# Kernel tuning notes

Hardware: AMD Instinct MI355X
Metric: run time of the kernel (lower is better)

## Reference

```python
import jax, jax.numpy as jnp
import numpy as np


def _pairwise_adj(x):
    # exp(-||xi - xj||^2), shape [B, N, N]
    inner = -2.0 * jnp.einsum('bnd,bmd->bnm', x, x)
    sq = jnp.sum(x * x, axis=-1, keepdims=True)
    return jnp.exp(-(sq + inner + jnp.swapaxes(sq, 1, 2)))


def _knn_adj(adj, k):
    # keep top-k weights per row, zero elsewhere
    vals, idx = jax.lax.top_k(adj, k)
    b = jnp.arange(adj.shape[0])[:, None, None]
    n = jnp.arange(adj.shape[1])[None, :, None]
    return jnp.zeros_like(adj).at[b, n, idx].set(vals)


def _laplacian(adj):
    # normalized Laplacian L = I - D^-1/2 A D^-1/2
    d = jnp.sum(adj, axis=-1)
    dinv = jnp.where(d > 0, 1.0 / jnp.sqrt(d), 0.0)
    norm_adj = dinv[:, :, None] * adj * dinv[:, None, :]
    return jnp.eye(adj.shape[1], dtype=adj.dtype) - norm_adj


def _cheb_conv(x, L, W, b):
    # Chebyshev polynomial graph conv: sum_k T_k(L) x W_k + b
    K = W.shape[0]
    x0 = x
    out = jnp.einsum('bnf,fo->bno', x0, W[0])
    if K > 1:
        x1 = jnp.matmul(L, x0)
        out = out + jnp.einsum('bnf,fo->bno', x1, W[1])
        for kk in range(2, K):
            x2 = 2.0 * jnp.matmul(L, x1) - x0
            out = out + jnp.einsum('bnf,fo->bno', x2, W[kk])
            x0, x1 = x1, x2
    return out + b


def setup_inputs() -> dict:
    key = jax.random.key(0)
    ks = jax.random.split(key, 4)
    B, N, Fin, Fout, K, C = 16, 2048, 6, 128, 6, 40
    x = jax.random.normal(ks[0], (B, N, Fin), dtype=jnp.float32)
    sccs = jax.random.randint(ks[1], (B, 64, 16), 0, N)  # unused in one_layer branch
    W1 = jax.random.normal(ks[2], (K, Fin, Fout), dtype=jnp.float32) * 0.05
    b1 = jnp.zeros((Fout,), dtype=jnp.float32)
    fc_w = jax.random.normal(ks[3], (Fout, C), dtype=jnp.float32) * 0.05
    fc_b = jnp.zeros((C,), dtype=jnp.float32)
    return {"x": x, "k": 40, "batch_size": B, "num_points": N,
            "sccs": sccs, "W1": W1, "b1": b1, "fc_w": fc_w, "fc_b": fc_b}


def reference(x, k, batch_size, num_points, sccs, W1, b1, fc_w, fc_b):
    # graph built under no_grad in the original -> stop_gradient here
    L = jax.lax.stop_gradient(_laplacian(_knn_adj(_pairwise_adj(x), k)))
    out = jax.nn.relu(_cheb_conv(x, L, W1, b1))           # [B, N, 128]
    # reg_prior: ||out^T L out||_F ** 2
    M = jnp.einsum('bnf,bnm,bmg->bfg', out, L, out)       # [B, 128, 128]
    reg = jnp.sum(M * M)
    pooled = jnp.max(out, axis=1)                         # [B, 128]
    logits = pooled @ fc_w + fc_b                         # [B, class_num]
    return logits, reg
```

## Files before the change

### kernel.cpp

```cpp
#include <hip/hip_runtime.h>
#include <math.h>

#define BB   16
#define NN   2048
#define FIN  6
#define FOUT 128
#define KCH  6
#define KNN  40
#define NCLS 40

__global__ __launch_bounds__(512) void knn_kernel(const float* __restrict__ x,
                                                  int* __restrict__ topi,
                                                  float* __restrict__ topv,
                                                  float* __restrict__ dinv)
{
    __shared__ __align__(16) float xs[FIN][NN];
    __shared__ unsigned int   hist[8][64];
    __shared__ unsigned int   ck[8][64];
    __shared__ unsigned short ci[8][64];
    __shared__ unsigned int   ccnt[8];

    int bb   = blockIdx.x >> 5;
    int i0   = (blockIdx.x & 31) * 64;
    int t    = threadIdx.x;
    int lane = t & 63;
    int wv   = t >> 6;

    const float* xb = x + (size_t)bb * NN * FIN;
    for (int idx = t; idx < NN * FIN; idx += 512) {
        int j = idx / FIN, f = idx - j * FIN;
        xs[f][j] = xb[idx];
    }
    __syncthreads();

    for (int rr = 0; rr < 8; ++rr) {
        int i   = i0 + wv * 8 + rr;
        int row = bb * NN + i;

        float xi0 = xs[0][i], xi1 = xs[1][i], xi2 = xs[2][i],
              xi3 = xs[3][i], xi4 = xs[4][i], xi5 = xs[5][i];

        float d[32];
#pragma unroll
        for (int uu = 0; uu < 8; ++uu) {
            int j4 = uu * 64 + lane;
            float4 p0 = ((const float4*)xs[0])[j4];
            float4 p1 = ((const float4*)xs[1])[j4];
            float4 p2 = ((const float4*)xs[2])[j4];
            float4 p3 = ((const float4*)xs[3])[j4];
            float4 p4 = ((const float4*)xs[4])[j4];
            float4 p5 = ((const float4*)xs[5])[j4];
#define DNE(E, C)                                                                \
            { float q0 = p0.C - xi0, q1 = p1.C - xi1, q2 = p2.C - xi2,           \
                    q3 = p3.C - xi3, q4 = p4.C - xi4, q5 = p5.C - xi5;           \
              d[uu * 4 + E] = fmaf(q5,q5, fmaf(q4,q4, fmaf(q3,q3,                \
                              fmaf(q2,q2, fmaf(q1,q1, q0*q0)))));  }
            DNE(0, x) DNE(1, y) DNE(2, z) DNE(3, w)
#undef DNE
        }

        float lo = 0.0f, invw = 16.0f;
        int base = 0, pivot = 127;

        for (int pass = 0; pass < 6; ++pass) {
            hist[wv][lane] = 0u;
#pragma unroll
            for (int u = 0; u < 32; ++u) {
                float dv = d[u];
                if (dv >= lo) {
                    int bin = (int)((dv - lo) * invw);
                    if (bin < 128)
                        atomicAdd(&hist[wv][bin >> 1], 1u << ((bin & 1) << 4));
                }
            }
            unsigned int h = hist[wv][lane];
            int b0 = (int)(h & 0xFFFFu), b1 = (int)(h >> 16);
            int s = b0 + b1;
            int incl = s;
#pragma unroll
            for (int off = 1; off < 64; off <<= 1) {
                int up = __shfl_up(incl, off, 64);
                if (lane >= off) incl += up;
            }
            int total = __shfl(incl, 63, 64);

            if (base + total < KNN) {
                base += total;
                lo   += 128.0f / invw;
                invw *= 0.5f;
                continue;
            }

            unsigned long long ball = __ballot(base + incl >= KNN);
            int pl = __ffsll(ball) - 1;
            int p_ = 0, cb_ = 0, cs_ = 0;
            if (lane == pl) {
                int cbefore = base + incl - s;
                if (cbefore + b0 >= KNN) { p_ = pl * 2;     cb_ = cbefore;      cs_ = cbefore + b0; }
                else                     { p_ = pl * 2 + 1; cb_ = cbefore + b0; cs_ = cbefore + b0 + b1; }
            }
            pivot    = __shfl(p_, pl, 64);
            int cumb = __shfl(cb_, pl, 64);
            int csel = __shfl(cs_, pl, 64);

            if (csel <= 64) break;

            lo   = lo + (float)pivot / invw;
            invw *= 128.0f;
            base = cumb;
        }

        if (lane == 0) ccnt[wv] = 0u;
#pragma unroll
        for (int u = 0; u < 32; ++u) {
            int ib = (int)((d[u] - lo) * invw);
            if (ib <= pivot) {
                unsigned int slot = atomicAdd(&ccnt[wv], 1u);
                if (slot < 64u) {
                    ck[wv][slot] = __float_as_uint(d[u]);
                    ci[wv][slot] = (unsigned short)((u >> 2) * 256 + (lane << 2) + (u & 3));
                }
            }
        }
        unsigned int c = ccnt[wv];
        if (c > 64u) c = 64u;

        unsigned int kk = (lane < (int)c) ? ck[wv][lane] : 0xFFFFFFFFu;
        int          id = (lane < (int)c) ? (int)ci[wv][lane] : -1;

        int rank = 0;
        int cI = (int)c;
        for (int m = 0; m < cI; ++m) {
            unsigned int km = __shfl(kk, m, 64);
            rank += (km < kk || (km == kk && m < lane)) ? 1 : 0;
        }

        float ev = 0.0f;
        if (rank < KNN) {
            ev = expf(-__uint_as_float(kk));
            topv[(size_t)row * KNN + rank] = ev;
            topi[(size_t)row * KNN + rank] = id;
        }
        float ssum = ev;
#pragma unroll
        for (int off = 32; off; off >>= 1) ssum += __shfl_xor(ssum, off, 64);
        if (lane == 0) dinv[row] = 1.0f / sqrtf(ssum);
    }
}

__global__ void weight_kernel(const int* __restrict__ topi,
                              const float* __restrict__ topv,
                              const float* __restrict__ dinv,
                              float* __restrict__ wnrm)
{
    int idx = blockIdx.x * 256 + threadIdx.x;
    if (idx >= BB * NN * KNN) return;
    int row = idx / KNN;
    int b   = row >> 11;
    int j   = topi[idx];
    wnrm[idx] = topv[idx] * dinv[row] * dinv[b * NN + j];
}

__global__ __launch_bounds__(192) void cheb_apply(const float* __restrict__ xin,
                                                  const float* __restrict__ xsub,
                                                  float* __restrict__ xout,
                                                  const int* __restrict__ topi,
                                                  const float* __restrict__ wnrm,
                                                  float scale)
{
    __shared__ int   si[32 * KNN];
    __shared__ float sw[32 * KNN];
    int r0 = blockIdx.x * 32;
    int t  = threadIdx.x;
    for (int l = t; l < 32 * KNN; l += 192) {
        si[l] = topi[(size_t)r0 * KNN + l];
        sw[l] = wnrm[(size_t)r0 * KNN + l];
    }
    __syncthreads();

    int rl = t / FIN, f = t - rl * FIN;
    int r  = r0 + rl;
    int b  = r >> 11;
    const float* xbase = xin + (size_t)b * NN * FIN + f;
    const int*   sip = si + rl * KNN;
    const float* swp = sw + rl * KNN;
    float a = xin[(size_t)r * FIN + f];
#pragma unroll 8
    for (int s = 0; s < KNN; ++s)
        a = fmaf(-swp[s], xbase[(size_t)sip[s] * FIN], a);
    a *= scale;
    if (xsub) a -= xsub[(size_t)r * FIN + f];
    xout[(size_t)r * FIN + f] = a;
}

__global__ __launch_bounds__(512) void chebout_kernel(const float* __restrict__ x,
                                                      const float* __restrict__ xks,
                                                      const float* __restrict__ W1,
                                                      const float* __restrict__ b1,
                                                      float* __restrict__ outb)
{
    __shared__ float W1s[KCH * FIN * FOUT];
    __shared__ float b1s[FOUT];
    __shared__ float xk[4][KCH * FIN];
    int r0 = blockIdx.x * 4;
    int t  = threadIdx.x;
    for (int l = t; l < KCH * FIN * FOUT; l += 512) W1s[l] = W1[l];
    if (t < FOUT) b1s[t] = b1[t];
    if (t < 4 * KCH * FIN) {
        int rl = t / (KCH * FIN), kf = t % (KCH * FIN);
        int k = kf / FIN, f = kf % FIN;
        int r = r0 + rl;
        xk[rl][kf] = (k == 0) ? x[(size_t)r * FIN + f]
                              : xks[(size_t)(k - 1) * BB * NN * FIN + (size_t)r * FIN + f];
    }
    __syncthreads();
    int rl = t >> 7, fo = t & 127;
    float acc = b1s[fo];
#pragma unroll
    for (int kf = 0; kf < KCH * FIN; ++kf)
        acc = fmaf(xk[rl][kf], W1s[kf * FOUT + fo], acc);
    outb[(size_t)(r0 + rl) * FOUT + fo] = fmaxf(acc, 0.0f);
}

__global__ __launch_bounds__(128) void lout_kernel(const float* __restrict__ outb,
                                                   const int* __restrict__ topi,
                                                   const float* __restrict__ wnrm,
                                                   float* __restrict__ lout)
{
    int id = blockIdx.x;
    int q  = id >> 3;
    int bb = (id & 7) + 8 * (q >> 11);
    int i  = q & 2047;
    int r  = bb * NN + i;
    int t  = threadIdx.x;
    __shared__ int   si[KNN];
    __shared__ float sw[KNN];
    if (t < KNN) { si[t] = topi[(size_t)r * KNN + t]; sw[t] = wnrm[(size_t)r * KNN + t]; }
    __syncthreads();
    const float* ob = outb + (size_t)bb * NN * FOUT;
    float acc = outb[(size_t)r * FOUT + t];
#pragma unroll 8
    for (int s = 0; s < KNN; ++s)
        acc -= sw[s] * ob[(size_t)si[s] * FOUT + t];
    lout[(size_t)r * FOUT + t] = acc;
}

__global__ __launch_bounds__(256) void msq_kernel(const float* __restrict__ outb,
                                                  const float* __restrict__ lout,
                                                  float* __restrict__ mchunk)
{
    int id   = blockIdx.x;
    int u    = id >> 3;
    int bb   = (id & 7) + 8 * (u >> 5);
    int rem  = u & 31;
    int tile = rem >> 3;
    int nch  = rem & 7;
    int tf0  = (tile & 1) * 64, tg0 = (tile >> 1) * 64;
    int t    = threadIdx.x;
    int tx   = t & 15, ty = t >> 4;
    __shared__ __align__(16) float aT[64][64];
    __shared__ __align__(16) float bT[64][64];
    const float* ob = outb + (size_t)bb * NN * FOUT + tf0;
    const float* lb = lout + (size_t)bb * NN * FOUT + tg0;
    float acc[4][4] = {{0.f}};
    for (int n0 = nch * 256; n0 < nch * 256 + 256; n0 += 64) {
        for (int l = t; l < 1024; l += 256) {
            int rr = l >> 4, c4 = (l & 15) << 2;
            *(float4*)&aT[rr][c4] = *(const float4*)&ob[(size_t)(n0 + rr) * FOUT + c4];
            *(float4*)&bT[rr][c4] = *(const float4*)&lb[(size_t)(n0 + rr) * FOUT + c4];
        }
        __syncthreads();
#pragma unroll 8
        for (int qq = 0; qq < 64; ++qq) {
            float4 av = *(const float4*)&aT[qq][tx * 4];
            float4 bv = *(const float4*)&bT[qq][ty * 4];
            float af[4] = {av.x, av.y, av.z, av.w};
            float bg[4] = {bv.x, bv.y, bv.z, bv.w};
#pragma unroll
            for (int ii = 0; ii < 4; ++ii)
#pragma unroll
                for (int jj = 0; jj < 4; ++jj)
                    acc[ii][jj] = fmaf(af[ii], bg[jj], acc[ii][jj]);
        }
        __syncthreads();
    }
    size_t basem = (size_t)(bb * 8 + nch) * (FOUT * FOUT);
#pragma unroll
    for (int ii = 0; ii < 4; ++ii) {
        float4 v = make_float4(acc[ii][0], acc[ii][1], acc[ii][2], acc[ii][3]);
        *(float4*)&mchunk[basem + (size_t)(tf0 + tx * 4 + ii) * FOUT + tg0 + ty * 4] = v;
    }
}

__global__ __launch_bounds__(256) void mred_kernel(const float* __restrict__ mchunk,
                                                   float* __restrict__ mpart)
{
    int t = threadIdx.x;
    size_t E = ((size_t)blockIdx.x * 256 + t) * 4;
    int bb = (int)(E >> 14);
    int fg = (int)(E & 16383);
    float4 a = make_float4(0.f, 0.f, 0.f, 0.f);
    for (int c = 0; c < 8; ++c) {
        float4 v = *(const float4*)&mchunk[((size_t)(bb * 8 + c) << 14) + fg];
        a.x += v.x; a.y += v.y; a.z += v.z; a.w += v.w;
    }
    float s = a.x * a.x + a.y * a.y + a.z * a.z + a.w * a.w;
#pragma unroll
    for (int off = 32; off; off >>= 1) s += __shfl_down(s, off, 64);
    __shared__ float ws[4];
    if ((t & 63) == 0) ws[t >> 6] = s;
    __syncthreads();
    if (t == 0) mpart[blockIdx.x] = ws[0] + ws[1] + ws[2] + ws[3];
}

__global__ __launch_bounds__(128) void pmax_kernel(const float* __restrict__ outb,
                                                   float* __restrict__ pmax)
{
    int c = blockIdx.x, b = blockIdx.y, t = threadIdx.x;
    const float* ob = outb + ((size_t)b * NN + (size_t)c * 128) * FOUT;
    float m = -3.0e38f;
#pragma unroll 4
    for (int n = 0; n < 128; ++n) m = fmaxf(m, ob[(size_t)n * FOUT + t]);
    pmax[((size_t)b * 16 + c) * FOUT + t] = m;
}

__global__ __launch_bounds__(128) void logits_kernel(const float* __restrict__ pmax,
                                                     const float* __restrict__ fcw,
                                                     const float* __restrict__ fcb,
                                                     float* __restrict__ dout)
{
    int b = blockIdx.x, t = threadIdx.x;
    __shared__ float pooled[FOUT];
    float m = pmax[((size_t)b * 16 + 0) * FOUT + t];
    for (int c = 1; c < 16; ++c) m = fmaxf(m, pmax[((size_t)b * 16 + c) * FOUT + t]);
    pooled[t] = m;
    __syncthreads();
    if (t < NCLS) {
        float acc = fcb[t];
        for (int f = 0; f < FOUT; ++f) acc = fmaf(pooled[f], fcw[f * NCLS + t], acc);
        dout[b * NCLS + t] = acc;
    }
}

__global__ __launch_bounds__(256) void reg_kernel(const float* __restrict__ mpart,
                                                  float* __restrict__ dout)
{
    int t = threadIdx.x;
    float s = mpart[t];
#pragma unroll
    for (int off = 32; off; off >>= 1) s += __shfl_down(s, off, 64);
    __shared__ float ws[4];
    if ((t & 63) == 0) ws[t >> 6] = s;
    __syncthreads();
    if (t == 0) dout[0] = ws[0] + ws[1] + ws[2] + ws[3];
}

extern "C" void kernel_launch(void* const* d_in, const int* in_sizes, int n_in,
                              void* d_out, int out_size, void* d_ws, size_t ws_size,
                              hipStream_t stream)
{
    const float* x   = (const float*)d_in[0];
    const float* W1  = (const float*)d_in[5];
    const float* b1  = (const float*)d_in[6];
    const float* fcw = (const float*)d_in[7];
    const float* fcb = (const float*)d_in[8];

    char* p = (char*)d_ws;
    auto alloc = [&](size_t bytes) { void* q = (void*)p; p += (bytes + 255) & ~(size_t)255; return q; };
    int*   topi   = (int*)  alloc((size_t)BB * NN * KNN * 4);
    float* topv   = (float*)alloc((size_t)BB * NN * KNN * 4);
    float* dinv   = (float*)alloc((size_t)BB * NN * 4);
    float* wnrm   = (float*)alloc((size_t)BB * NN * KNN * 4);
    float* xks    = (float*)alloc((size_t)5 * BB * NN * FIN * 4);
    float* outb   = (float*)alloc((size_t)BB * NN * FOUT * 4);
    float* lout   = (float*)alloc((size_t)BB * NN * FOUT * 4);
    float* mchunk = (float*)alloc((size_t)BB * 8 * FOUT * FOUT * 4);
    float* mpart  = (float*)alloc(256 * 4);
    float* pmax   = (float*)alloc((size_t)BB * 16 * FOUT * 4);

    const size_t ST = (size_t)BB * NN * FIN;

    knn_kernel<<<512, 512, 0, stream>>>(x, topi, topv, dinv);
    weight_kernel<<<(BB * NN * KNN + 255) / 256, 256, 0, stream>>>(topi, topv, dinv, wnrm);

    cheb_apply<<<1024, 192, 0, stream>>>(x,            nullptr,      xks + 0 * ST, topi, wnrm, 1.0f);
    cheb_apply<<<1024, 192, 0, stream>>>(xks + 0 * ST, x,            xks + 1 * ST, topi, wnrm, 2.0f);
    cheb_apply<<<1024, 192, 0, stream>>>(xks + 1 * ST, xks + 0 * ST, xks + 2 * ST, topi, wnrm, 2.0f);
    cheb_apply<<<1024, 192, 0, stream>>>(xks + 2 * ST, xks + 1 * ST, xks + 3 * ST, topi, wnrm, 2.0f);
    cheb_apply<<<1024, 192, 0, stream>>>(xks + 3 * ST, xks + 2 * ST, xks + 4 * ST, topi, wnrm, 2.0f);

    chebout_kernel<<<BB * NN / 4, 512, 0, stream>>>(x, xks, W1, b1, outb);
    lout_kernel<<<BB * NN, 128, 0, stream>>>(outb, topi, wnrm, lout);
    msq_kernel<<<512, 256, 0, stream>>>(outb, lout, mchunk);
    mred_kernel<<<256, 256, 0, stream>>>(mchunk, mpart);
    pmax_kernel<<<dim3(16, 16), 128, 0, stream>>>(outb, pmax);
    logits_kernel<<<BB, 128, 0, stream>>>(pmax, fcw, fcb, (float*)d_out);
    reg_kernel<<<1, 256, 0, stream>>>(mpart, (float*)d_out + BB * NCLS);
}
```

Before: 255.0 us.

## Fuse weight normalization into first Chebyshev pass and L*out into M computation

Removes the separate weight_kernel by computing normalized edge weights in the first cheb_apply launch, which also writes them out for later passes. The lout and msq kernels are merged into a single 1024-thread kernel that computes each L*out tile in shared memory and immediately accumulates out^T(L out), so the lout buffer never goes through global memory. chebout now handles 16 rows per block so each W1 shared-memory load is reused across more rows. The trade-off is fewer, larger blocks (256 in the fused kernel) and twice as many M partial chunks for mred to reduce.

```diff
diff --git a/kernel.cpp b/kernel.cpp
--- a/kernel.cpp
+++ b/kernel.cpp
@@ -148,33 +148,35 @@
     }
 }
 
-__global__ void weight_kernel(const int* __restrict__ topi,
-                              const float* __restrict__ topv,
-                              const float* __restrict__ dinv,
-                              float* __restrict__ wnrm)
-{
-    int idx = blockIdx.x * 256 + threadIdx.x;
-    if (idx >= BB * NN * KNN) return;
-    int row = idx / KNN;
-    int b   = row >> 11;
-    int j   = topi[idx];
-    wnrm[idx] = topv[idx] * dinv[row] * dinv[b * NN + j];
-}
-
 __global__ __launch_bounds__(192) void cheb_apply(const float* __restrict__ xin,
                                                   const float* __restrict__ xsub,
                                                   float* __restrict__ xout,
                                                   const int* __restrict__ topi,
                                                   const float* __restrict__ wnrm,
+                                                  const float* __restrict__ topv,
+                                                  const float* __restrict__ dinv,
+                                                  float* __restrict__ wnrm_out,
                                                   float scale)
 {
     __shared__ int   si[32 * KNN];
     __shared__ float sw[32 * KNN];
     int r0 = blockIdx.x * 32;
     int t  = threadIdx.x;
-    for (int l = t; l < 32 * KNN; l += 192) {
-        si[l] = topi[(size_t)r0 * KNN + l];
-        sw[l] = wnrm[(size_t)r0 * KNN + l];
+    if (topv) {
+        int b = r0 >> 11;
+        const float* dv = dinv + ((size_t)b << 11);
+        for (int l = t; l < 32 * KNN; l += 192) {
+            size_t idx = (size_t)r0 * KNN + l;
+            int j = topi[idx];
+            float w = topv[idx] * dinv[r0 + l / KNN] * dv[j];
+            si[l] = j; sw[l] = w;
+            wnrm_out[idx] = w;
+        }
+    } else {
+        for (int l = t; l < 32 * KNN; l += 192) {
+            si[l] = topi[(size_t)r0 * KNN + l];
+            sw[l] = wnrm[(size_t)r0 * KNN + l];
+        }
     }
     __syncthreads();
 
@@ -201,79 +203,84 @@
 {
     __shared__ float W1s[KCH * FIN * FOUT];
     __shared__ float b1s[FOUT];
-    __shared__ float xk[4][KCH * FIN];
-    int r0 = blockIdx.x * 4;
+    __shared__ float xk[16][KCH * FIN];
+    int r0 = blockIdx.x * 16;
     int t  = threadIdx.x;
     for (int l = t; l < KCH * FIN * FOUT; l += 512) W1s[l] = W1[l];
     if (t < FOUT) b1s[t] = b1[t];
-    if (t < 4 * KCH * FIN) {
-        int rl = t / (KCH * FIN), kf = t % (KCH * FIN);
+    for (int l = t; l < 16 * KCH * FIN; l += 512) {
+        int rl = l / (KCH * FIN), kf = l % (KCH * FIN);
         int k = kf / FIN, f = kf % FIN;
         int r = r0 + rl;
         xk[rl][kf] = (k == 0) ? x[(size_t)r * FIN + f]
                               : xks[(size_t)(k - 1) * BB * NN * FIN + (size_t)r * FIN + f];
     }
     __syncthreads();
-    int rl = t >> 7, fo = t & 127;
-    float acc = b1s[fo];
-#pragma unroll
-    for (int kf = 0; kf < KCH * FIN; ++kf)
-        acc = fmaf(xk[rl][kf], W1s[kf * FOUT + fo], acc);
-    outb[(size_t)(r0 + rl) * FOUT + fo] = fmaxf(acc, 0.0f);
-}
-
-__global__ __launch_bounds__(128) void lout_kernel(const float* __restrict__ outb,
-                                                   const int* __restrict__ topi,
-                                                   const float* __restrict__ wnrm,
-                                                   float* __restrict__ lout)
-{
-    int id = blockIdx.x;
-    int q  = id >> 3;
-    int bb = (id & 7) + 8 * (q >> 11);
-    int i  = q & 2047;
-    int r  = bb * NN + i;
-    int t  = threadIdx.x;
-    __shared__ int   si[KNN];
-    __shared__ float sw[KNN];
-    if (t < KNN) { si[t] = topi[(size_t)r * KNN + t]; sw[t] = wnrm[(size_t)r * KNN + t]; }
-    __syncthreads();
+    int fo = t & 127;
+#pragma unroll
+    for (int it = 0; it < 4; ++it) {
+        int rl = (t >> 7) + it * 4;
+        float acc = b1s[fo];
+#pragma unroll
+        for (int kf = 0; kf < KCH * FIN; ++kf)
+            acc = fmaf(xk[rl][kf], W1s[kf * FOUT + fo], acc);
+        outb[(size_t)(r0 + rl) * FOUT + fo] = fmaxf(acc, 0.0f);
+    }
+}
+
+__global__ __launch_bounds__(1024) void loutmsq_kernel(const float* __restrict__ outb,
+                                                       const int* __restrict__ topi,
+                                                       const float* __restrict__ wnrm,
+                                                       float* __restrict__ mchunk)
+{
+    int id  = blockIdx.x;
+    int xcd = id & 7, k = id >> 3;
+    int bb  = xcd + 8 * (k >> 4);
+    int nch = k & 15;
+    int t   = threadIdx.x;
+
+    __shared__ __align__(16) float aT[64][FOUT];
+    __shared__ __align__(16) float bT[64][FOUT];
+
     const float* ob = outb + (size_t)bb * NN * FOUT;
-    float acc = outb[(size_t)r * FOUT + t];
+    float acc[4][4] = {{0.f}};
+    int tx = t & 31, ty = t >> 5;
+    int grl = t >> 4;
+    int gfq = (t & 15) * 2;
+
+    for (int st = 0; st < 2; ++st) {
+        int n0 = nch * 128 + st * 64;
+        {
+            const float4* src = (const float4*)(ob + (size_t)n0 * FOUT);
+            float4* dst = (float4*)aT;
+            dst[t]        = src[t];
+            dst[t + 1024] = src[t + 1024];
+        }
+        __syncthreads();
+        {
+            int r = n0 + grl;
+            const int*   ti = topi + ((size_t)bb * NN + r) * KNN;
+            const float* tw = wnrm + ((size_t)bb * NN + r) * KNN;
+            float4 a0 = ((const float4*)aT[grl])[gfq];
+            float4 a1 = ((const float4*)aT[grl])[gfq + 1];
 #pragma unroll 8
-    for (int s = 0; s < KNN; ++s)
-        acc -= sw[s] * ob[(size_t)si[s] * FOUT + t];
-    lout[(size_t)r * FOUT + t] = acc;
-}
-
-__global__ __launch_bounds__(256) void msq_kernel(const float* __restrict__ outb,
-                                                  const float* __restrict__ lout,
-                                                  float* __restrict__ mchunk)
-{
-    int id   = blockIdx.x;
-    int u    = id >> 3;
-    int bb   = (id & 7) + 8 * (u >> 5);
-    int rem  = u & 31;
-    int tile = rem >> 3;
-    int nch  = rem & 7;
-    int tf0  = (tile & 1) * 64, tg0 = (tile >> 1) * 64;
-    int t    = threadIdx.x;
-    int tx   = t & 15, ty = t >> 4;
-    __shared__ __align__(16) float aT[64][64];
-    __shared__ __align__(16) float bT[64][64];
-    const float* ob = outb + (size_t)bb * NN * FOUT + tf0;
-    const float* lb = lout + (size_t)bb * NN * FOUT + tg0;
-    float acc[4][4] = {{0.f}};
-    for (int n0 = nch * 256; n0 < nch * 256 + 256; n0 += 64) {
-        for (int l = t; l < 1024; l += 256) {
-            int rr = l >> 4, c4 = (l & 15) << 2;
-            *(float4*)&aT[rr][c4] = *(const float4*)&ob[(size_t)(n0 + rr) * FOUT + c4];
-            *(float4*)&bT[rr][c4] = *(const float4*)&lb[(size_t)(n0 + rr) * FOUT + c4];
+            for (int s = 0; s < KNN; ++s) {
+                int j = ti[s]; float w = tw[s];
+                const float4* jr = (const float4*)(ob + (size_t)j * FOUT);
+                float4 v0 = jr[gfq], v1 = jr[gfq + 1];
+                a0.x = fmaf(-w, v0.x, a0.x); a0.y = fmaf(-w, v0.y, a0.y);
+                a0.z = fmaf(-w, v0.z, a0.z); a0.w = fmaf(-w, v0.w, a0.w);
+                a1.x = fmaf(-w, v1.x, a1.x); a1.y = fmaf(-w, v1.y, a1.y);
+                a1.z = fmaf(-w, v1.z, a1.z); a1.w = fmaf(-w, v1.w, a1.w);
+            }
+            ((float4*)bT[grl])[gfq]     = a0;
+            ((float4*)bT[grl])[gfq + 1] = a1;
         }
         __syncthreads();
 #pragma unroll 8
         for (int qq = 0; qq < 64; ++qq) {
-            float4 av = *(const float4*)&aT[qq][tx * 4];
-            float4 bv = *(const float4*)&bT[qq][ty * 4];
+            float4 av = ((const float4*)aT[qq])[tx];
+            float4 bv = ((const float4*)bT[qq])[ty];
             float af[4] = {av.x, av.y, av.z, av.w};
             float bg[4] = {bv.x, bv.y, bv.z, bv.w};
 #pragma unroll
@@ -284,11 +291,11 @@
         }
         __syncthreads();
     }
-    size_t basem = (size_t)(bb * 8 + nch) * (FOUT * FOUT);
+    size_t basem = ((size_t)bb * 16 + nch) << 14;
 #pragma unroll
     for (int ii = 0; ii < 4; ++ii) {
         float4 v = make_float4(acc[ii][0], acc[ii][1], acc[ii][2], acc[ii][3]);
-        *(float4*)&mchunk[basem + (size_t)(tf0 + tx * 4 + ii) * FOUT + tg0 + ty * 4] = v;
+        *(float4*)&mchunk[basem + (size_t)(tx * 4 + ii) * FOUT + ty * 4] = v;
     }
 }
 
@@ -300,8 +307,8 @@
     int bb = (int)(E >> 14);
     int fg = (int)(E & 16383);
     float4 a = make_float4(0.f, 0.f, 0.f, 0.f);
-    for (int c = 0; c < 8; ++c) {
-        float4 v = *(const float4*)&mchunk[((size_t)(bb * 8 + c) << 14) + fg];
+    for (int c = 0; c < 16; ++c) {
+        float4 v = *(const float4*)&mchunk[((size_t)(bb * 16 + c) << 14) + fg];
         a.x += v.x; a.y += v.y; a.z += v.z; a.w += v.w;
     }
     float s = a.x * a.x + a.y * a.y + a.z * a.z + a.w * a.w;
@@ -373,25 +380,22 @@
     float* wnrm   = (float*)alloc((size_t)BB * NN * KNN * 4);
     float* xks    = (float*)alloc((size_t)5 * BB * NN * FIN * 4);
     float* outb   = (float*)alloc((size_t)BB * NN * FOUT * 4);
-    float* lout   = (float*)alloc((size_t)BB * NN * FOUT * 4);
-    float* mchunk = (float*)alloc((size_t)BB * 8 * FOUT * FOUT * 4);
+    float* mchunk = (float*)alloc((size_t)BB * 16 * FOUT * FOUT * 4);
     float* mpart  = (float*)alloc(256 * 4);
     float* pmax   = (float*)alloc((size_t)BB * 16 * FOUT * 4);
 
     const size_t ST = (size_t)BB * NN * FIN;
 
     knn_kernel<<<512, 512, 0, stream>>>(x, topi, topv, dinv);
-    weight_kernel<<<(BB * NN * KNN + 255) / 256, 256, 0, stream>>>(topi, topv, dinv, wnrm);
-
-    cheb_apply<<<1024, 192, 0, stream>>>(x,            nullptr,      xks + 0 * ST, topi, wnrm, 1.0f);
-    cheb_apply<<<1024, 192, 0, stream>>>(xks + 0 * ST, x,            xks + 1 * ST, topi, wnrm, 2.0f);
-    cheb_apply<<<1024, 192, 0, stream>>>(xks + 1 * ST, xks + 0 * ST, xks + 2 * ST, topi, wnrm, 2.0f);
-    cheb_apply<<<1024, 192, 0, stream>>>(xks + 2 * ST, xks + 1 * ST, xks + 3 * ST, topi, wnrm, 2.0f);
-    cheb_apply<<<1024, 192, 0, stream>>>(xks + 3 * ST, xks + 2 * ST, xks + 4 * ST, topi, wnrm, 2.0f);
-
-    chebout_kernel<<<BB * NN / 4, 512, 0, stream>>>(x, xks, W1, b1, outb);
-    lout_kernel<<<BB * NN, 128, 0, stream>>>(outb, topi, wnrm, lout);
-    msq_kernel<<<512, 256, 0, stream>>>(outb, lout, mchunk);
+
+    cheb_apply<<<1024, 192, 0, stream>>>(x,            nullptr,      xks + 0 * ST, topi, nullptr, topv, dinv, wnrm, 1.0f);
+    cheb_apply<<<1024, 192, 0, stream>>>(xks + 0 * ST, x,            xks + 1 * ST, topi, wnrm, nullptr, nullptr, nullptr, 2.0f);
+    cheb_apply<<<1024, 192, 0, stream>>>(xks + 1 * ST, xks + 0 * ST, xks + 2 * ST, topi, wnrm, nullptr, nullptr, nullptr, 2.0f);
+    cheb_apply<<<1024, 192, 0, stream>>>(xks + 2 * ST, xks + 1 * ST, xks + 3 * ST, topi, wnrm, nullptr, nullptr, nullptr, 2.0f);
+    cheb_apply<<<1024, 192, 0, stream>>>(xks + 3 * ST, xks + 2 * ST, xks + 4 * ST, topi, wnrm, nullptr, nullptr, nullptr, 2.0f);
+
+    chebout_kernel<<<BB * NN / 16, 512, 0, stream>>>(x, xks, W1, b1, outb);
+    loutmsq_kernel<<<256, 1024, 0, stream>>>(outb, topi, wnrm, mchunk);
     mred_kernel<<<256, 256, 0, stream>>>(mchunk, mpart);
     pmax_kernel<<<dim3(16, 16), 128, 0, stream>>>(outb, pmax);
     logits_kernel<<<BB, 128, 0, stream>>>(pmax, fcw, fcb, (float*)d_out);
```

Result: faster. 240.6 us (-5.7%).
